# Kernel tuning notes

Measured on AMD Instinct MI355X. Metric: run time of the kernel, lower is better.

Reference implementation:

```python
import jax, jax.numpy as jnp
import numpy as np

N_NODES = 100000
N_EDGES = 1600000
NODE_F = 25
HID = 128
LN_EPS = 1e-5


def _mlp_ln(h, w1, b1, w2, b2, w3, b3, g, beta):
    # Linear -> ReLU -> Linear -> ReLU -> Linear -> LayerNorm
    h = jax.nn.relu(h @ w1 + b1)
    h = jax.nn.relu(h @ w2 + b2)
    h = h @ w3 + b3
    mu = jnp.mean(h, axis=-1, keepdims=True)
    var = jnp.mean(jnp.square(h - mu), axis=-1, keepdims=True)
    return (h - mu) * jax.lax.rsqrt(var + LN_EPS) * g + beta


def setup_inputs() -> dict:
    key = jax.random.key(0)
    ks = jax.random.split(key, 10)
    x = jax.random.normal(ks[0], (N_NODES, NODE_F), dtype=jnp.float32)
    edge_index = jax.random.randint(ks[1], (2, N_EDGES), 0, N_NODES, dtype=jnp.int64)

    def lin(k, fin, fout):
        s = 1.0 / np.sqrt(fin)
        kw, kb = jax.random.split(k)
        w = jax.random.uniform(kw, (fin, fout), jnp.float32, -s, s)
        b = jax.random.uniform(kb, (fout,), jnp.float32, -s, s)
        return w, b

    ew1, eb1 = lin(ks[2], 4, HID)
    ew2, eb2 = lin(ks[3], HID, HID)
    ew3, eb3 = lin(ks[4], HID, HID)
    nw1, nb1 = lin(ks[5], NODE_F, HID)
    nw2, nb2 = lin(ks[6], HID, HID)
    nw3, nb3 = lin(ks[7], HID, HID)
    eg = jnp.ones((HID,), jnp.float32); ebeta = jnp.zeros((HID,), jnp.float32)
    ng = jnp.ones((HID,), jnp.float32); nbeta = jnp.zeros((HID,), jnp.float32)
    return dict(x=x, edge_index=edge_index,
                ew1=ew1, eb1=eb1, ew2=ew2, eb2=eb2, ew3=ew3, eb3=eb3, eg=eg, ebeta=ebeta,
                nw1=nw1, nb1=nb1, nw2=nw2, nb2=nb2, nw3=nw3, nb3=nb3, ng=ng, nbeta=nbeta)


def reference(x, edge_index, ew1, eb1, ew2, eb2, ew3, eb3, eg, ebeta,
              nw1, nb1, nw2, nb2, nw3, nb3, ng, nbeta):
    row, col = edge_index[0], edge_index[1]
    # edge model: gather src/dest positions, relative displacement + magnitude
    distance = x[row, 0:3] - x[col, 0:3]                      # [E, 3]
    magnitude = jnp.linalg.norm(distance, axis=1, keepdims=True)  # [E, 1]
    edge_in = jnp.concatenate([distance, magnitude], axis=1)  # [E, 4]
    edge_out = _mlp_ln(edge_in, ew1, eb1, ew2, eb2, ew3, eb3, eg, ebeta)  # [E, 128]
    # node model: MLP over raw x (the masked copy in the original is unused)
    node_out = _mlp_ln(x, nw1, nb1, nw2, nb2, nw3, nb3, ng, nbeta)  # [N, 128]
    return node_out, edge_out
```

## Files before the change

### kernel.cpp

```cpp
#include <hip/hip_runtime.h>

#define E_EDGES 1600000
#define N_NODES_ 100000

typedef unsigned short u16;
typedef unsigned int u32;
typedef short bf16x8 __attribute__((ext_vector_type(8)));
typedef u16 u16x4 __attribute__((ext_vector_type(4)));
typedef float f32x4 __attribute__((ext_vector_type(4)));

#define BAR() do{ asm volatile("s_waitcnt lgkmcnt(0)" ::: "memory"); \
                  __builtin_amdgcn_s_barrier(); }while(0)

__device__ __forceinline__ u16 f2bf(float f){
  u32 u = __builtin_bit_cast(u32, f);
  u += 0x7fffu + ((u >> 16) & 1u);
  return (u16)(u >> 16);
}

__global__ void pack4(const float* __restrict__ a, const float* __restrict__ b,
                      const float* __restrict__ c, const float* __restrict__ d,
                      u16* __restrict__ pa, u16* __restrict__ pb,
                      u16* __restrict__ pc, u16* __restrict__ pd){
  int tid = blockIdx.x * 256 + threadIdx.x;
  int mat = tid >> 11, rem = tid & 2047;
  int n = rem >> 8, k = (rem >> 6) & 3, lane = rem & 63;
  const float* w = mat==0 ? a : mat==1 ? b : mat==2 ? c : d;
  u16* p       = mat==0 ? pa : mat==1 ? pb : mat==2 ? pc : pd;
  int rbase = k*32 + (lane>>4)*8;
  int col   = n*16 + (lane&15);
  int o = ((n*4 + k)*64 + lane)*8;
  #pragma unroll
  for (int j=0;j<8;++j) p[o+j] = f2bf(w[(rbase+j)*128 + col]);
}

__global__ void pack_xyz(const float* __restrict__ x, float4* __restrict__ xyz, int n){
  int i = blockIdx.x * 256 + threadIdx.x;
  if (i < n){
    const float* p = x + (long)i*25;
    float4 v; v.x = p[0]; v.y = p[1]; v.z = p[2]; v.w = 0.f;
    xyz[i] = v;
  }
}

template<int IS_EDGE>
__global__ __launch_bounds__(256, 4)
void encoder_kernel(const float* __restrict__ x, const int* __restrict__ eidx,
                    const float4* __restrict__ xyz,
                    const float* __restrict__ w1, const float* __restrict__ b1,
                    const u16* __restrict__ pw2, const float* __restrict__ b2,
                    const u16* __restrict__ pw3, const float* __restrict__ b3,
                    const float* __restrict__ gw, const float* __restrict__ bw,
                    float* __restrict__ out, long outbase, int nrows, int ntiles)
{
  constexpr int K1  = IS_EDGE ? 4 : 25;
  constexpr int K1P = IS_EDGE ? 4 : 26;
  constexpr int WGS = K1*32 + 4;
  constexpr int SP  = 132;

  __shared__ __align__(16) float w1s[4*WGS];
  __shared__ __align__(16) float b1s[4*36];
  __shared__ __align__(16) float in_s[64*K1P];
  __shared__ __align__(16) unsigned char h12s[16384];
  __shared__ __align__(16) float pts[64*8];
  float* stage = (float*)h12s;

  const int tid  = threadIdx.x;
  const int lane = tid & 63, wave = tid >> 6;
  const int li = lane & 15, lg = lane >> 4;
  const int wbase = wave * 32;

  bf16x8 W2f[2][4], W3f[2][4];
  #pragma unroll
  for (int mt=0;mt<2;++mt)
    #pragma unroll
    for (int kc=0;kc<4;++kc){
      W2f[mt][kc] = *(const bf16x8*)(pw2 + (((wave*2+mt)*4 + kc)*64 + lane)*8);
      W3f[mt][kc] = *(const bf16x8*)(pw3 + (((wave*2+mt)*4 + kc)*64 + lane)*8);
    }
  f32x4 b2q[2];
  #pragma unroll
  for (int mt=0;mt<2;++mt)
    b2q[mt] = *(const f32x4*)(b2 + wbase + mt*16 + lg*4);
  asm volatile("" ::: "memory");

  for (int i = tid; i < K1*32; i += 256){
    int k = i >> 5, col = (i & 31) * 4;
    float4 v = ((const float4*)w1)[i];
    *(float4*)(w1s + (col>>5)*WGS + k*32 + (col&31)) = v;
  }
  if (tid < 128) b1s[(tid>>5)*36 + (tid&31)] = b1[tid];

  float4 curg = {0.f,0.f,0.f,0.f};
  int ni0 = 0, ni1 = 0;
  float4 nr4 = {0.f,0.f,0.f,0.f}, nc4 = {0.f,0.f,0.f,0.f};
  if (IS_EDGE && tid < 64){
    int t0 = blockIdx.x;
    if (t0 < ntiles){
      long e = (long)t0*64 + tid;
      int ir = eidx[e], ic = eidx[E_EDGES + e];
      float4 a = xyz[ir], b = xyz[ic];
      float dx = a.x-b.x, dy = a.y-b.y, dz = a.z-b.z;
      curg.x=dx; curg.y=dy; curg.z=dz; curg.w=sqrtf(dx*dx+dy*dy+dz*dz);
      int t1 = t0 + gridDim.x;
      if (t1 < ntiles){
        long e1 = (long)t1*64 + tid;
        ni0 = eidx[e1]; ni1 = eidx[E_EDGES + e1];
      }
    }
  }

  const f32x4 zv = {0.f,0.f,0.f,0.f};

  for (int tile = blockIdx.x; tile < ntiles; tile += gridDim.x){
    const int row0 = tile * 64;
    const bool hasnext = (tile + (int)gridDim.x) < ntiles;

    if (IS_EDGE){
      if (tid < 64){
        ((float4*)in_s)[tid] = curg;
        if (hasnext){
          nr4 = xyz[ni0]; nc4 = xyz[ni1];
          int t2 = tile + 2*(int)gridDim.x;
          if (t2 < ntiles){
            long e2 = (long)t2*64 + tid;
            ni0 = eidx[e2]; ni1 = eidx[E_EDGES + e2];
          }
        }
      }
    } else {
      for (int i = tid; i < 64*25; i += 256){
        int r = i / 25, k = i - r*25;
        float v = (row0 + r < nrows) ? x[(long)row0*25 + i] : 0.f;
        in_s[r*K1P + k] = v;
      }
    }
    BAR();

    {
      const int r = tid >> 2, jb0 = (tid & 3) << 5;
      #pragma unroll
      for (int p=0;p<2;++p){
        const int jb = jb0 + p*16;
        const int g = jb >> 5, go = jb & 31;
        float a1[16];
        #pragma unroll
        for (int j=0;j<16;++j) a1[j] = b1s[g*36 + go + j];
        for (int k=0;k<K1;++k){
          float xv = in_s[r*K1P + k];
          const float4* wr = (const float4*)(w1s + g*WGS + k*32 + go);
          #pragma unroll
          for (int j4=0;j4<4;++j4){
            float4 wv = wr[j4];
            a1[j4*4+0] = fmaf(xv, wv.x, a1[j4*4+0]);
            a1[j4*4+1] = fmaf(xv, wv.y, a1[j4*4+1]);
            a1[j4*4+2] = fmaf(xv, wv.z, a1[j4*4+2]);
            a1[j4*4+3] = fmaf(xv, wv.w, a1[j4*4+3]);
          }
        }
        #pragma unroll
        for (int q=0;q<2;++q){
          bf16x8 pk;
          #pragma unroll
          for (int t=0;t<8;++t){
            float v = a1[q*8+t]; v = v > 0.f ? v : 0.f;
            pk[t] = (short)f2bf(v);
          }
          *(bf16x8*)(h12s + r*256 + ((((jb>>3)+q) ^ (r&7))<<4)) = pk;
        }
      }
    }
    BAR();

    f32x4 acc[2][4];
    #pragma unroll
    for (int mt=0;mt<2;++mt)
      #pragma unroll
      for (int nt=0;nt<4;++nt) acc[mt][nt] = zv;
    #pragma unroll
    for (int kc=0;kc<4;++kc){
      #pragma unroll
      for (int nt=0;nt<4;++nt){
        bf16x8 hf = *(const bf16x8*)(h12s + (nt*16+li)*256 + (((kc*4+lg)^(li&7))<<4));
        acc[0][nt] = __builtin_amdgcn_mfma_f32_16x16x32_bf16(W2f[0][kc], hf, acc[0][nt], 0,0,0);
        acc[1][nt] = __builtin_amdgcn_mfma_f32_16x16x32_bf16(W2f[1][kc], hf, acc[1][nt], 0,0,0);
      }
    }

    if (IS_EDGE && tid < 64 && hasnext){
      float dx = nr4.x-nc4.x, dy = nr4.y-nc4.y, dz = nr4.z-nc4.z;
      curg.x=dx; curg.y=dy; curg.z=dz; curg.w=sqrtf(dx*dx+dy*dy+dz*dz);
    }

    BAR();

    #pragma unroll
    for (int mt=0;mt<2;++mt){
      const int f0 = wbase + mt*16 + lg*4;
      #pragma unroll
      for (int nt=0;nt<4;++nt){
        u16x4 pk;
        #pragma unroll
        for (int j=0;j<4;++j){
          float v = acc[mt][nt][j] + b2q[mt][j];
          v = v > 0.f ? v : 0.f;
          pk[j] = f2bf(v);
        }
        const int r = nt*16 + li;
        *(u16x4*)(h12s + r*256 + (((f0>>3) ^ (r&7))<<4) + ((f0&7)<<1)) = pk;
      }
    }
    BAR();

    #pragma unroll
    for (int mt=0;mt<2;++mt)
      #pragma unroll
      for (int nt=0;nt<4;++nt) acc[mt][nt] = zv;
    #pragma unroll
    for (int kc=0;kc<4;++kc){
      #pragma unroll
      for (int nt=0;nt<4;++nt){
        bf16x8 hf = *(const bf16x8*)(h12s + (nt*16+li)*256 + (((kc*4+lg)^(li&7))<<4));
        acc[0][nt] = __builtin_amdgcn_mfma_f32_16x16x32_bf16(W3f[0][kc], hf, acc[0][nt], 0,0,0);
        acc[1][nt] = __builtin_amdgcn_mfma_f32_16x16x32_bf16(W3f[1][kc], hf, acc[1][nt], 0,0,0);
      }
    }

    f32x4 b3q[2], gq[2], bq[2];
    #pragma unroll
    for (int mt=0;mt<2;++mt){
      b3q[mt] = *(const f32x4*)(b3 + wbase + mt*16 + lg*4);
      gq[mt]  = *(const f32x4*)(gw + wbase + mt*16 + lg*4);
      bq[mt]  = *(const f32x4*)(bw + wbase + mt*16 + lg*4);
    }

    float sA[4]  = {0.f,0.f,0.f,0.f};
    float sqA[4] = {0.f,0.f,0.f,0.f};
    #pragma unroll
    for (int mt=0;mt<2;++mt)
      #pragma unroll
      for (int nt=0;nt<4;++nt)
        #pragma unroll
        for (int j=0;j<4;++j){
          float v = acc[mt][nt][j] + b3q[mt][j];
          acc[mt][nt][j] = v;
          sA[nt] += v; sqA[nt] += v*v;
        }
    #pragma unroll
    for (int nt=0;nt<4;++nt){
      sA[nt]  += __shfl_xor(sA[nt], 16);  sA[nt]  += __shfl_xor(sA[nt], 32);
      sqA[nt] += __shfl_xor(sqA[nt], 16); sqA[nt] += __shfl_xor(sqA[nt], 32);
    }
    if (lg == 0){
      #pragma unroll
      for (int nt=0;nt<4;++nt){
        pts[(nt*16+li)*8 + wave*2]     = sA[nt];
        pts[(nt*16+li)*8 + wave*2 + 1] = sqA[nt];
      }
    }
    BAR();

    #pragma unroll
    for (int nt=0;nt<4;++nt){
      {
        const int r = nt*16 + li;
        f32x4 p0 = *(const f32x4*)(pts + r*8);
        f32x4 p1 = *(const f32x4*)(pts + r*8 + 4);
        float S  = p0[0]+p0[2]+p1[0]+p1[2];
        float SQ = p0[1]+p0[3]+p1[1]+p1[3];
        float mu = S * 0.0078125f;
        float rs = rsqrtf(SQ*0.0078125f - mu*mu + 1e-5f);
        #pragma unroll
        for (int mt=0;mt<2;++mt){
          f32x4 o;
          #pragma unroll
          for (int j=0;j<4;++j)
            o[j] = (acc[mt][nt][j]-mu)*rs*gq[mt][j] + bq[mt][j];
          *(f32x4*)(stage + li*SP + wbase + mt*16 + lg*4) = o;
        }
      }
      BAR();
      #pragma unroll
      for (int i=0;i<2;++i){
        const int r = i*8 + (tid>>5);
        const int c = (tid&31)*4;
        const int grow = row0 + nt*16 + r;
        float4 v = *(const float4*)(stage + r*SP + c);
        if (IS_EDGE || grow < nrows)
          *(float4*)(out + outbase + (long)grow*128 + c) = v;
      }
      if (nt < 3) BAR();
    }
  }
}

extern "C" void kernel_launch(void* const* d_in, const int* in_sizes, int n_in,
                              void* d_out, int out_size, void* d_ws, size_t ws_size,
                              hipStream_t stream){
  const float* x   = (const float*)d_in[0];
  const int*  eidx = (const int*)d_in[1];
  const float* ew1 = (const float*)d_in[2];
  const float* eb1 = (const float*)d_in[3];
  const float* ew2 = (const float*)d_in[4];
  const float* eb2 = (const float*)d_in[5];
  const float* ew3 = (const float*)d_in[6];
  const float* eb3 = (const float*)d_in[7];
  const float* eg  = (const float*)d_in[8];
  const float* ebt = (const float*)d_in[9];
  const float* nw1 = (const float*)d_in[10];
  const float* nb1 = (const float*)d_in[11];
  const float* nw2 = (const float*)d_in[12];
  const float* nb2 = (const float*)d_in[13];
  const float* nw3 = (const float*)d_in[14];
  const float* nb3 = (const float*)d_in[15];
  const float* ng  = (const float*)d_in[16];
  const float* nbt = (const float*)d_in[17];
  float* out = (float*)d_out;

  u16* pew2 = (u16*)d_ws;
  u16* pew3 = pew2 + 16384;
  u16* pnw2 = pew3 + 16384;
  u16* pnw3 = pnw2 + 16384;
  float4* xyz = (float4*)((char*)d_ws + 131072);

  pack4<<<32, 256, 0, stream>>>(ew2, ew3, nw2, nw3, pew2, pew3, pnw2, pnw3);
  pack_xyz<<<(N_NODES_ + 255)/256, 256, 0, stream>>>(x, xyz, N_NODES_);
  encoder_kernel<1><<<1792, 256, 0, stream>>>(x, eidx, xyz, ew1, eb1, pew2, eb2, pew3, eb3,
      eg, ebt, out, (long)N_NODES_ * 128, E_EDGES, E_EDGES/64);
  encoder_kernel<0><<<1024, 256, 0, stream>>>(x, nullptr, nullptr, nw1, nb1, pnw2, nb2, pnw3, nb3,
      ng, nbt, out, 0, N_NODES_, (N_NODES_ + 63)/64);
}
```

Measured before the change: 542.5 us.

## Add wave-independent edge kernel with LDS-resident weights and register layer-1

Replaces the edge path of the shared encoder with a dedicated kernel in which each wave independently handles 16 edges. Layer-1 runs directly in registers as MFMA A-operands, and the packed W2/W3 weights sit in LDS shared by 16 waves. LayerNorm statistics come from cross-lane shuffles and the output is transposed through shuffles, so the per-tile block barriers disappear. The cost is a large LDS footprint (about 132KB per 1024-thread block), which limits occupancy, and B-fragments are re-read from LDS for every subtile.

Result: faster. 485.6 us (-10.5%).

```diff
diff --git a/kernel.cpp b/kernel.cpp
--- a/kernel.cpp
+++ b/kernel.cpp
@@ -43,6 +43,185 @@
   }
 }
 
+__global__ __launch_bounds__(1024, 4)
+void edge_kernel(const int* __restrict__ eidx, const float4* __restrict__ xyz,
+                 const float* __restrict__ w1, const float* __restrict__ b1,
+                 const u16* __restrict__ pw2, const float* __restrict__ b2,
+                 const u16* __restrict__ pw3, const float* __restrict__ b3,
+                 const float* __restrict__ gw, const float* __restrict__ bw,
+                 float* __restrict__ out, long outbase)
+{
+  __shared__ __align__(16) u16 W2L[16384];
+  __shared__ __align__(16) u16 W3L[16384];
+  __shared__ __align__(16) float w1s[4*132];
+  __shared__ __align__(16) float b1L[128];
+  __shared__ __align__(16) unsigned char h2buf[16*4096];
+
+  const int tid  = threadIdx.x;
+  const int lane = tid & 63, wave = tid >> 6;
+  const int li = lane & 15, lg = lane >> 4;
+  unsigned char* h2 = h2buf + wave*4096;
+
+  for (int i = tid; i < 2048; i += 1024){
+    ((float4*)W2L)[i] = ((const float4*)pw2)[i];
+    ((float4*)W3L)[i] = ((const float4*)pw3)[i];
+  }
+  for (int i = tid; i < 512; i += 1024){
+    int k = i >> 7, f = i & 127;
+    w1s[k*132 + f] = w1[i];
+  }
+  if (tid < 128) b1L[tid] = b1[tid];
+  __syncthreads();
+
+  float b2v[8], b3v[8], gv[8], bv[8];
+  #pragma unroll
+  for (int n=0;n<8;++n){
+    int f = li + n*16;
+    b2v[n] = b2[f]; b3v[n] = b3[f]; gv[n] = gw[f]; bv[n] = bw[f];
+  }
+
+  const int NSUB = E_EDGES/16;
+  const int wid = blockIdx.x*16 + wave;
+  const int stride = gridDim.x*16;
+  const f32x4 zv = {0.f,0.f,0.f,0.f};
+
+  float4 pr = {0,0,0,0}, pc = {0,0,0,0};
+  if (wid < NSUB){
+    long e = (long)wid*16 + li;
+    int ir = eidx[e], ic = eidx[E_EDGES + e];
+    pr = xyz[ir]; pc = xyz[ic];
+  }
+
+  for (int s = wid; s < NSUB; s += stride){
+    float dx = pr.x-pc.x, dy = pr.y-pc.y, dz = pr.z-pc.z;
+    float4 in4; in4.x = dx; in4.y = dy; in4.z = dz;
+    in4.w = sqrtf(dx*dx + dy*dy + dz*dz);
+
+    int sn = s + stride;
+    if (sn < NSUB){
+      long e = (long)sn*16 + li;
+      int ir = eidx[e], ic = eidx[E_EDGES + e];
+      pr = xyz[ir]; pc = xyz[ic];
+    }
+
+    bf16x8 af[4];
+    #pragma unroll
+    for (int kc=0;kc<4;++kc){
+      const int f0 = kc*32 + lg*8;
+      f32x4 bA = *(const f32x4*)(b1L + f0);
+      f32x4 bB = *(const f32x4*)(b1L + f0 + 4);
+      float h[8];
+      #pragma unroll
+      for (int j=0;j<4;++j){ h[j] = bA[j]; h[4+j] = bB[j]; }
+      #pragma unroll
+      for (int k=0;k<4;++k){
+        float xv = (k==0)?in4.x:(k==1)?in4.y:(k==2)?in4.z:in4.w;
+        f32x4 wa = *(const f32x4*)(w1s + k*132 + f0);
+        f32x4 wb = *(const f32x4*)(w1s + k*132 + f0 + 4);
+        #pragma unroll
+        for (int j=0;j<4;++j){
+          h[j]   = fmaf(xv, wa[j], h[j]);
+          h[4+j] = fmaf(xv, wb[j], h[4+j]);
+        }
+      }
+      #pragma unroll
+      for (int j=0;j<8;++j){
+        float v = h[j] > 0.f ? h[j] : 0.f;
+        af[kc][j] = (short)f2bf(v);
+      }
+    }
+
+    f32x4 acc[8];
+    #pragma unroll
+    for (int n=0;n<8;++n) acc[n] = zv;
+    #pragma unroll
+    for (int n=0;n<8;++n)
+      #pragma unroll
+      for (int kc=0;kc<4;++kc){
+        bf16x8 bf = *(const bf16x8*)(W2L + ((n*4+kc)*64 + lane)*8);
+        acc[n] = __builtin_amdgcn_mfma_f32_16x16x32_bf16(af[kc], bf, acc[n], 0,0,0);
+      }
+
+    #pragma unroll
+    for (int n=0;n<8;++n){
+      #pragma unroll
+      for (int j=0;j<4;++j){
+        float v = acc[n][j] + b2v[n];
+        v = v > 0.f ? v : 0.f;
+        const int rr = lg*4 + j;
+        const int f  = li + n*16;
+        *(u16*)(h2 + rr*256 + ((((f>>3)) ^ (rr&7))<<4) + ((f&7)<<1)) = f2bf(v);
+      }
+    }
+    asm volatile("s_waitcnt lgkmcnt(0)" ::: "memory");
+    __builtin_amdgcn_sched_barrier(0);
+
+    bf16x8 a2[4];
+    #pragma unroll
+    for (int kc=0;kc<4;++kc)
+      a2[kc] = *(const bf16x8*)(h2 + li*256 + (((kc*4+lg) ^ (li&7))<<4));
+    #pragma unroll
+    for (int n=0;n<8;++n) acc[n] = zv;
+    #pragma unroll
+    for (int n=0;n<8;++n)
+      #pragma unroll
+      for (int kc=0;kc<4;++kc){
+        bf16x8 bf = *(const bf16x8*)(W3L + ((n*4+kc)*64 + lane)*8);
+        acc[n] = __builtin_amdgcn_mfma_f32_16x16x32_bf16(a2[kc], bf, acc[n], 0,0,0);
+      }
+
+    float sj[4] = {0,0,0,0}, qj[4] = {0,0,0,0};
+    #pragma unroll
+    for (int n=0;n<8;++n)
+      #pragma unroll
+      for (int j=0;j<4;++j){
+        float v = acc[n][j] + b3v[n];
+        acc[n][j] = v;
+        sj[j] += v; qj[j] += v*v;
+      }
+    #pragma unroll
+    for (int j=0;j<4;++j){
+      sj[j] += __shfl_xor(sj[j],1);  qj[j] += __shfl_xor(qj[j],1);
+      sj[j] += __shfl_xor(sj[j],2);  qj[j] += __shfl_xor(qj[j],2);
+      sj[j] += __shfl_xor(sj[j],4);  qj[j] += __shfl_xor(qj[j],4);
+      sj[j] += __shfl_xor(sj[j],8);  qj[j] += __shfl_xor(qj[j],8);
+    }
+    float mu[4], rs[4];
+    #pragma unroll
+    for (int j=0;j<4;++j){
+      mu[j] = sj[j] * 0.0078125f;
+      rs[j] = rsqrtf(qj[j]*0.0078125f - mu[j]*mu[j] + 1e-5f);
+    }
+    #pragma unroll
+    for (int n=0;n<8;++n)
+      #pragma unroll
+      for (int j=0;j<4;++j)
+        acc[n][j] = (acc[n][j]-mu[j])*rs[j]*gv[n] + bv[n];
+
+    const int t = li & 3;
+    const long rowb = outbase + (long)(s*16)*128;
+    #pragma unroll
+    for (int n=0;n<8;++n){
+      float a0 = acc[n][0], a1 = acc[n][1], a2f = acc[n][2], a3 = acc[n][3];
+      float s0 = __shfl_xor(a1,1), s1 = __shfl_xor(a0,1);
+      float s2 = __shfl_xor(a3,1), s3 = __shfl_xor(a2f,1);
+      float c0 = (t&1) ? s0 : a0;
+      float c1 = (t&1) ? a1 : s1;
+      float c2 = (t&1) ? s2 : a2f;
+      float c3 = (t&1) ? a3 : s3;
+      float u0 = __shfl_xor(c2,2), u1 = __shfl_xor(c3,2);
+      float u2 = __shfl_xor(c0,2), u3 = __shfl_xor(c1,2);
+      float4 o;
+      o.x = (t&2) ? u0 : c0;
+      o.y = (t&2) ? u1 : c1;
+      o.z = (t&2) ? c2 : u2;
+      o.w = (t&2) ? c3 : u3;
+      float* op = out + rowb + (long)(lg*4 + t)*128 + (li>>2)*4 + n*16;
+      *(float4*)op = o;
+    }
+  }
+}
+
 template<int IS_EDGE>
 __global__ __launch_bounds__(256, 4)
 void encoder_kernel(const float* __restrict__ x, const int* __restrict__ eidx,
@@ -91,49 +270,14 @@
   }
   if (tid < 128) b1s[(tid>>5)*36 + (tid&31)] = b1[tid];
 
-  float4 curg = {0.f,0.f,0.f,0.f};
-  int ni0 = 0, ni1 = 0;
-  float4 nr4 = {0.f,0.f,0.f,0.f}, nc4 = {0.f,0.f,0.f,0.f};
-  if (IS_EDGE && tid < 64){
-    int t0 = blockIdx.x;
-    if (t0 < ntiles){
-      long e = (long)t0*64 + tid;
-      int ir = eidx[e], ic = eidx[E_EDGES + e];
-      float4 a = xyz[ir], b = xyz[ic];
-      float dx = a.x-b.x, dy = a.y-b.y, dz = a.z-b.z;
-      curg.x=dx; curg.y=dy; curg.z=dz; curg.w=sqrtf(dx*dx+dy*dy+dz*dz);
-      int t1 = t0 + gridDim.x;
-      if (t1 < ntiles){
-        long e1 = (long)t1*64 + tid;
-        ni0 = eidx[e1]; ni1 = eidx[E_EDGES + e1];
-      }
-    }
-  }
-
   const f32x4 zv = {0.f,0.f,0.f,0.f};
 
   for (int tile = blockIdx.x; tile < ntiles; tile += gridDim.x){
     const int row0 = tile * 64;
-    const bool hasnext = (tile + (int)gridDim.x) < ntiles;
-
-    if (IS_EDGE){
-      if (tid < 64){
-        ((float4*)in_s)[tid] = curg;
-        if (hasnext){
-          nr4 = xyz[ni0]; nc4 = xyz[ni1];
-          int t2 = tile + 2*(int)gridDim.x;
-          if (t2 < ntiles){
-            long e2 = (long)t2*64 + tid;
-            ni0 = eidx[e2]; ni1 = eidx[E_EDGES + e2];
-          }
-        }
-      }
-    } else {
-      for (int i = tid; i < 64*25; i += 256){
-        int r = i / 25, k = i - r*25;
-        float v = (row0 + r < nrows) ? x[(long)row0*25 + i] : 0.f;
-        in_s[r*K1P + k] = v;
-      }
+    for (int i = tid; i < 64*25; i += 256){
+      int r = i / 25, k = i - r*25;
+      float v = (row0 + r < nrows) ? x[(long)row0*25 + i] : 0.f;
+      in_s[r*K1P + k] = v;
     }
     BAR();
 
@@ -162,9 +306,9 @@
         for (int q=0;q<2;++q){
           bf16x8 pk;
           #pragma unroll
-          for (int t=0;t<8;++t){
-            float v = a1[q*8+t]; v = v > 0.f ? v : 0.f;
-            pk[t] = (short)f2bf(v);
+          for (int t2=0;t2<8;++t2){
+            float v = a1[q*8+t2]; v = v > 0.f ? v : 0.f;
+            pk[t2] = (short)f2bf(v);
           }
           *(bf16x8*)(h12s + r*256 + ((((jb>>3)+q) ^ (r&7))<<4)) = pk;
         }
@@ -186,12 +330,6 @@
         acc[1][nt] = __builtin_amdgcn_mfma_f32_16x16x32_bf16(W2f[1][kc], hf, acc[1][nt], 0,0,0);
       }
     }
-
-    if (IS_EDGE && tid < 64 && hasnext){
-      float dx = nr4.x-nc4.x, dy = nr4.y-nc4.y, dz = nr4.z-nc4.z;
-      curg.x=dx; curg.y=dy; curg.z=dz; curg.w=sqrtf(dx*dx+dy*dy+dz*dz);
-    }
-
     BAR();
 
     #pragma unroll
@@ -269,13 +407,13 @@
         float S  = p0[0]+p0[2]+p1[0]+p1[2];
         float SQ = p0[1]+p0[3]+p1[1]+p1[3];
         float mu = S * 0.0078125f;
-        float rs = rsqrtf(SQ*0.0078125f - mu*mu + 1e-5f);
+        float rsv = rsqrtf(SQ*0.0078125f - mu*mu + 1e-5f);
         #pragma unroll
         for (int mt=0;mt<2;++mt){
           f32x4 o;
           #pragma unroll
           for (int j=0;j<4;++j)
-            o[j] = (acc[mt][nt][j]-mu)*rs*gq[mt][j] + bq[mt][j];
+            o[j] = (acc[mt][nt][j]-mu)*rsv*gq[mt][j] + bq[mt][j];
           *(f32x4*)(stage + li*SP + wbase + mt*16 + lg*4) = o;
         }
       }
@@ -286,7 +424,7 @@
         const int c = (tid&31)*4;
         const int grow = row0 + nt*16 + r;
         float4 v = *(const float4*)(stage + r*SP + c);
-        if (IS_EDGE || grow < nrows)
+        if (grow < nrows)
           *(float4*)(out + outbase + (long)grow*128 + c) = v;
       }
       if (nt < 3) BAR();
@@ -325,8 +463,8 @@
 
   pack4<<<32, 256, 0, stream>>>(ew2, ew3, nw2, nw3, pew2, pew3, pnw2, pnw3);
   pack_xyz<<<(N_NODES_ + 255)/256, 256, 0, stream>>>(x, xyz, N_NODES_);
-  encoder_kernel<1><<<1792, 256, 0, stream>>>(x, eidx, xyz, ew1, eb1, pew2, eb2, pew3, eb3,
-      eg, ebt, out, (long)N_NODES_ * 128, E_EDGES, E_EDGES/64);
+  edge_kernel<<<256, 1024, 0, stream>>>(eidx, xyz, ew1, eb1, pew2, eb2, pew3, eb3,
+      eg, ebt, out, (long)N_NODES_ * 128);
   encoder_kernel<0><<<1024, 256, 0, stream>>>(x, nullptr, nullptr, nw1, nb1, pnw2, nb2, pnw3, nb3,
       ng, nbt, out, 0, N_NODES_, (N_NODES_ + 63)/64);
 }
```
